# Performance work log

Measured on AMD Instinct MI355X. Metric: run time of the kernel, lower is better.

The kernel has to match this reference:

```python
import jax, jax.numpy as jnp
import numpy as np

N_NODES = 50000
EPS = 1e-12  # F.normalize eps


def _gcn_layer(x, W, b, src, dst):
    # GCNConv(normalize=False): h = x @ W, then sum-aggregate messages from
    # source nodes into target nodes along edge_index, then add bias.
    h = x @ W
    agg = jax.ops.segment_sum(h[src], dst, num_segments=N_NODES)
    out = agg + b
    # F.normalize(p=2, dim=-1) then ReLU
    norm = jnp.linalg.norm(out, axis=-1, keepdims=True)
    out = out / jnp.maximum(norm, EPS)
    return jax.nn.relu(out)


def setup_inputs() -> dict:
    key = jax.random.key(0)
    ks = jax.random.split(key, 8)
    nfeat, nhid, nclass, n_edges = 128, 128, 40, 640000
    x = jax.random.normal(ks[0], (N_NODES, nfeat), dtype=jnp.float32)
    edge_index = jax.random.randint(ks[1], (2, n_edges), 0, N_NODES, dtype=jnp.int64)
    s = 1.0 / np.sqrt(nhid)
    return {
        "x": x,
        "edge_index": edge_index,
        "W1": jax.random.normal(ks[2], (nfeat, nhid), jnp.float32) * s,
        "b1": jnp.zeros((nhid,), jnp.float32),
        "W2": jax.random.normal(ks[3], (nhid, nhid), jnp.float32) * s,
        "b2": jnp.zeros((nhid,), jnp.float32),
        "W3": jax.random.normal(ks[4], (nhid, nhid), jnp.float32) * s,
        "b3": jnp.zeros((nhid,), jnp.float32),
        "W4": jax.random.normal(ks[5], (nhid, nhid), jnp.float32) * s,
        "b4": jnp.zeros((nhid,), jnp.float32),
        "Wl": jax.random.normal(ks[6], (nhid, nclass), jnp.float32) * s,
        "bl": jnp.zeros((nclass,), jnp.float32),
    }


def reference(x, edge_index, W1, b1, W2, b2, W3, b3, W4, b4, Wl, bl):
    src, dst = edge_index[0], edge_index[1]
    x1 = _gcn_layer(x, W1, b1, src, dst)
    x2 = _gcn_layer(x1, W2, b2, src, dst)
    x3 = _gcn_layer(x2, W3, b3, src, dst)
    x4 = _gcn_layer(x3, W4, b4, src, dst)
    logits = x4 @ Wl + bl
    probs = jax.nn.softmax(logits, axis=-1)
    return (logits, probs, x4)
```

## Files before the change

### kernel.cpp

```cpp
#include <hip/hip_runtime.h>
#include <hip/hip_bf16.h>
#include <hip/hip_fp16.h>
#include <math.h>

#define NFEAT 128
#define NCLASS 40

typedef __attribute__((ext_vector_type(8))) short frag_ab;
typedef __attribute__((ext_vector_type(4))) float frag_cd;

static __device__ inline unsigned short f2bf_rne(float f) {
    union { float f; unsigned u; } v;
    v.f = f;
    unsigned r = v.u + 0x7FFFu + ((v.u >> 16) & 1u);
    return (unsigned short)(r >> 16);
}
static __device__ inline float bf2f(unsigned short h) {
    union { unsigned u; float f; } v;
    v.u = ((unsigned)h) << 16;
    return v.f;
}


__global__ __launch_bounds__(256) void prep_kernel(const float* __restrict__ x,
                                                   __half* __restrict__ xh, int xc4,
                                                   const float* __restrict__ W0,
                                                   const float* __restrict__ W1,
                                                   const float* __restrict__ W2,
                                                   const float* __restrict__ W3,
                                                   short* __restrict__ whi,
                                                   short* __restrict__ wlo,
                                                   const int* __restrict__ dst,
                                                   int* __restrict__ cnt, int n_edges,
                                                   int convB) {
    int b = blockIdx.x;
    if (b < convB) {
        int i = b * 256 + threadIdx.x;
        if (i < xc4) {
            float4 v = ((const float4*)x)[i];
            ((__half2*)xh)[i * 2 + 0] = __floats2half2_rn(v.x, v.y);
            ((__half2*)xh)[i * 2 + 1] = __floats2half2_rn(v.z, v.w);
        }
    } else if (b < convB + 32) {
        int wb = b - convB;
        int layer = wb >> 3;
        const float* W = layer == 0 ? W0 : layer == 1 ? W1 : layer == 2 ? W2 : W3;
        short* h = whi + (size_t)layer * 16384;
        short* l = wlo + (size_t)layer * 16384;
        int idx = (wb & 7) * 256 + threadIdx.x;
        int lane = idx & 63;
        int t = (idx >> 6) & 7;
        int s = idx >> 9;
        int quad = lane >> 4;
        int n = lane & 15;
        int kbase = s * 32 + quad * 8;
        int col = t * 16 + n;
#pragma unroll
        for (int j = 0; j < 8; ++j) {
            float f = W[(size_t)(kbase + j) * NFEAT + col];
            unsigned short hb = f2bf_rne(f);
            unsigned short lb = f2bf_rne(f - bf2f(hb));
            h[(size_t)idx * 8 + j] = (short)hb;
            l[(size_t)idx * 8 + j] = (short)lb;
        }
    } else {
        int hb = b - convB - 32;
        int i = hb * 256 + threadIdx.x;
        int n4 = n_edges >> 2;
        if (i < n4) {
            int4 d = ((const int4*)dst)[i];
            atomicAdd(&cnt[d.x], 1);
            atomicAdd(&cnt[d.y], 1);
            atomicAdd(&cnt[d.z], 1);
            atomicAdd(&cnt[d.w], 1);
        }
        if (hb == 0 && threadIdx.x == 0) {
            for (int e = n4 << 2; e < n_edges; ++e) atomicAdd(&cnt[dst[e]], 1);
        }
    }
}


__global__ __launch_bounds__(256) void scan1_kernel(const int* __restrict__ cnt,
                                                    int* __restrict__ excl,
                                                    int* __restrict__ bsums, int n) {
    __shared__ int sd[256];
    int t = threadIdx.x;
    int i = blockIdx.x * 256 + t;
    int v = (i < n) ? cnt[i] : 0;
    sd[t] = v;
    __syncthreads();
#pragma unroll
    for (int off = 1; off < 256; off <<= 1) {
        int tmp = (t >= off) ? sd[t - off] : 0;
        __syncthreads();
        sd[t] += tmp;
        __syncthreads();
    }
    if (i < n) excl[i] = sd[t] - v;
    if (t == 255) bsums[blockIdx.x] = sd[255];
}

__global__ __launch_bounds__(256) void scan3_kernel(const int* __restrict__ excl,
                                                    const int* __restrict__ bsums,
                                                    int* __restrict__ row_ptr,
                                                    int* __restrict__ woff, int n, int nb) {
    __shared__ int sd[256];
    __shared__ int off_s, tot_s;
    int t = threadIdx.x;
    int v = (t < nb) ? bsums[t] : 0;
    sd[t] = v;
    __syncthreads();
#pragma unroll
    for (int off = 1; off < 256; off <<= 1) {
        int tmp = (t >= off) ? sd[t - off] : 0;
        __syncthreads();
        sd[t] += tmp;
        __syncthreads();
    }
    if (t == 0) {
        off_s = (blockIdx.x > 0) ? sd[blockIdx.x - 1] : 0;
        tot_s = sd[255];
    }
    __syncthreads();
    int i = blockIdx.x * 256 + t;
    if (i < n) {
        int val = excl[i] + off_s;
        row_ptr[i] = val;
        woff[i] = val;
    }
    if (i == 0) row_ptr[n] = tot_s;
}

__global__ __launch_bounds__(256) void scatter_kernel(const int* __restrict__ src,
                                                      const int* __restrict__ dst,
                                                      int* __restrict__ woff,
                                                      int* __restrict__ src_sorted, int n_edges) {
    int i = blockIdx.x * 256 + threadIdx.x;
    int n4 = n_edges >> 2;
    if (i < n4) {
        int4 d = ((const int4*)dst)[i];
        int4 s = ((const int4*)src)[i];
        int p0 = atomicAdd(&woff[d.x], 1);
        int p1 = atomicAdd(&woff[d.y], 1);
        int p2 = atomicAdd(&woff[d.z], 1);
        int p3 = atomicAdd(&woff[d.w], 1);
        src_sorted[p0] = s.x;
        src_sorted[p1] = s.y;
        src_sorted[p2] = s.z;
        src_sorted[p3] = s.w;
    }
    if (i == 0) {
        for (int e = n4 << 2; e < n_edges; ++e) {
            int p = atomicAdd(&woff[dst[e]], 1);
            src_sorted[p] = src[e];
        }
    }
}


__global__ __launch_bounds__(256) void gcn_fused_kernel(const __half* __restrict__ xin,
                                                        const int* __restrict__ row_ptr,
                                                        const int* __restrict__ src_sorted,
                                                        const short* __restrict__ whi,
                                                        const short* __restrict__ wlo,
                                                        const float* __restrict__ bias,
                                                        float* __restrict__ outf,
                                                        __half* __restrict__ outh, int M) {
    __shared__ float smem[64][132];
    __shared__ int ctr;
    int tid = threadIdx.x;
    int base = blockIdx.x * 64;
    if (tid == 0) ctr = 0;
    __syncthreads();

    {
        int c = tid & 15;
        int lane = tid & 63;
        const uint4* xp = (const uint4*)xin;
        for (;;) {
            int nl = 0;
            if ((lane & 15) == 0) nl = atomicAdd(&ctr, 1);
            nl = __shfl(nl, lane & 48);
            if (nl >= 64) break;
            int node = base + nl;
            float a[8];
#pragma unroll
            for (int i = 0; i < 8; ++i) a[i] = 0.f;
            int jb = 0, je = 0;
            if (node < M) { jb = row_ptr[node]; je = row_ptr[node + 1]; }
            int j = jb;
            for (; j + 3 < je; j += 4) {
                int s0 = src_sorted[j];
                int s1 = src_sorted[j + 1];
                int s2 = src_sorted[j + 2];
                int s3 = src_sorted[j + 3];
                uint4 r0 = xp[s0 * 16 + c];
                uint4 r1 = xp[s1 * 16 + c];
                uint4 r2 = xp[s2 * 16 + c];
                uint4 r3 = xp[s3 * 16 + c];
#pragma unroll
                for (int q = 0; q < 4; ++q) {
                    unsigned u0 = (&r0.x)[q], u1 = (&r1.x)[q], u2 = (&r2.x)[q], u3 = (&r3.x)[q];
                    float2 f0 = __half22float2(*(__half2*)&u0);
                    float2 f1 = __half22float2(*(__half2*)&u1);
                    float2 f2 = __half22float2(*(__half2*)&u2);
                    float2 f3 = __half22float2(*(__half2*)&u3);
                    a[q * 2 + 0] += f0.x + f1.x + f2.x + f3.x;
                    a[q * 2 + 1] += f0.y + f1.y + f2.y + f3.y;
                }
            }
            for (; j < je; ++j) {
                int s0 = src_sorted[j];
                uint4 r0 = xp[s0 * 16 + c];
#pragma unroll
                for (int q = 0; q < 4; ++q) {
                    unsigned u0 = (&r0.x)[q];
                    float2 f0 = __half22float2(*(__half2*)&u0);
                    a[q * 2 + 0] += f0.x;
                    a[q * 2 + 1] += f0.y;
                }
            }
            float4* wp = (float4*)&smem[nl][c * 8];
            wp[0] = make_float4(a[0], a[1], a[2], a[3]);
            wp[1] = make_float4(a[4], a[5], a[6], a[7]);
        }
    }
    __syncthreads();

    int wave = tid >> 6;
    int lane = tid & 63;
    int quad = lane >> 4;
    int n16 = lane & 15;
    int lrow = wave * 16 + n16;

    const frag_ab* WH = (const frag_ab*)whi;
    const frag_ab* WL = (const frag_ab*)wlo;

    frag_cd acc[8];
#pragma unroll
    for (int t = 0; t < 8; ++t) acc[t] = (frag_cd){0.f, 0.f, 0.f, 0.f};

#pragma unroll
    for (int s = 0; s < 4; ++s) {
        const float* ap = &smem[lrow][s * 32 + quad * 8];
        float4 v0 = *(const float4*)(ap);
        float4 v1 = *(const float4*)(ap + 4);
        float fv[8] = {v0.x, v0.y, v0.z, v0.w, v1.x, v1.y, v1.z, v1.w};
        frag_ab ah, al;
#pragma unroll
        for (int jj = 0; jj < 8; ++jj) {
            unsigned short hb = f2bf_rne(fv[jj]);
            ah[jj] = (short)hb;
            al[jj] = (short)f2bf_rne(fv[jj] - bf2f(hb));
        }
#pragma unroll
        for (int t = 0; t < 8; ++t) {
            frag_ab bh = WH[(s * 8 + t) * 64 + lane];
            frag_ab bl = WL[(s * 8 + t) * 64 + lane];
            acc[t] = __builtin_amdgcn_mfma_f32_16x16x32_bf16(ah, bh, acc[t], 0, 0, 0);
            acc[t] = __builtin_amdgcn_mfma_f32_16x16x32_bf16(ah, bl, acc[t], 0, 0, 0);
            acc[t] = __builtin_amdgcn_mfma_f32_16x16x32_bf16(al, bh, acc[t], 0, 0, 0);
        }
    }

    float ssq[4] = {0.f, 0.f, 0.f, 0.f};
#pragma unroll
    for (int t = 0; t < 8; ++t) {
        float bv = bias[t * 16 + n16];
#pragma unroll
        for (int r = 0; r < 4; ++r) {
            acc[t][r] += bv;
            ssq[r] += acc[t][r] * acc[t][r];
        }
    }
#pragma unroll
    for (int mask = 1; mask <= 8; mask <<= 1) {
#pragma unroll
        for (int r = 0; r < 4; ++r) ssq[r] += __shfl_xor(ssq[r], mask);
    }
    float inv[4];
#pragma unroll
    for (int r = 0; r < 4; ++r) inv[r] = 1.0f / fmaxf(sqrtf(ssq[r]), 1e-12f);

    int orow0 = base + wave * 16 + quad * 4;
#pragma unroll
    for (int r = 0; r < 4; ++r) {
        int orow = orow0 + r;
        if (orow < M) {
            if (outh) {
                __half* op = outh + (size_t)orow * NFEAT + n16;
#pragma unroll
                for (int t = 0; t < 8; ++t)
                    op[t * 16] = __float2half(fmaxf(acc[t][r] * inv[r], 0.f));
            } else {
                float* op = outf + (size_t)orow * NFEAT + n16;
#pragma unroll
                for (int t = 0; t < 8; ++t)
                    op[t * 16] = fmaxf(acc[t][r] * inv[r], 0.f);
            }
        }
    }
}


__global__ __launch_bounds__(256) void classifier_kernel(const float* __restrict__ x4,
                                                         const float* __restrict__ Wl,
                                                         const float* __restrict__ bl,
                                                         float* __restrict__ logits,
                                                         float* __restrict__ probs, int n_nodes) {
    int node = blockIdx.x * 256 + threadIdx.x;
    int nc = node < n_nodes ? node : n_nodes - 1;
    const float* row = x4 + (size_t)nc * NFEAT;

    float acc[NCLASS];
#pragma unroll
    for (int c = 0; c < NCLASS; ++c) acc[c] = bl[c];

    for (int k = 0; k < NFEAT; k += 4) {
        float4 a = *(const float4*)(row + k);
#pragma unroll
        for (int kk = 0; kk < 4; ++kk) {
            float av = (&a.x)[kk];
            const float* Wr = Wl + (k + kk) * NCLASS;
#pragma unroll
            for (int c = 0; c < NCLASS; ++c) acc[c] += av * Wr[c];
        }
    }

    float m = acc[0];
#pragma unroll
    for (int c = 1; c < NCLASS; ++c) m = fmaxf(m, acc[c]);
    float ex[NCLASS];
    float sum = 0.f;
#pragma unroll
    for (int c = 0; c < NCLASS; ++c) {
        ex[c] = __expf(acc[c] - m);
        sum += ex[c];
    }
    float is = 1.0f / sum;

    if (node < n_nodes) {
        float4* lo = (float4*)(logits + (size_t)node * NCLASS);
        float4* po = (float4*)(probs + (size_t)node * NCLASS);
#pragma unroll
        for (int c = 0; c < NCLASS; c += 4) {
            float4 lv, pv;
            lv.x = acc[c + 0]; lv.y = acc[c + 1]; lv.z = acc[c + 2]; lv.w = acc[c + 3];
            pv.x = ex[c + 0] * is; pv.y = ex[c + 1] * is; pv.z = ex[c + 2] * is; pv.w = ex[c + 3] * is;
            lo[c >> 2] = lv;
            po[c >> 2] = pv;
        }
    }
}


extern "C" void kernel_launch(void* const* d_in, const int* in_sizes, int n_in,
                              void* d_out, int out_size, void* d_ws, size_t ws_size,
                              hipStream_t stream) {
    const float* x  = (const float*)d_in[0];
    const int*   ei = (const int*)d_in[1];
    const float* W1 = (const float*)d_in[2];
    const float* b1 = (const float*)d_in[3];
    const float* W2 = (const float*)d_in[4];
    const float* b2 = (const float*)d_in[5];
    const float* W3 = (const float*)d_in[6];
    const float* b3 = (const float*)d_in[7];
    const float* W4 = (const float*)d_in[8];
    const float* b4 = (const float*)d_in[9];
    const float* Wl = (const float*)d_in[10];
    const float* bl = (const float*)d_in[11];

    const int n_nodes = in_sizes[0] / NFEAT;
    const int n_edges = in_sizes[1] / 2;
    const int* src = ei;
    const int* dst = ei + n_edges;

    float* out    = (float*)d_out;
    float* logits = out;
    float* probs  = out + (size_t)n_nodes * NCLASS;
    float* x4     = out + 2 * (size_t)n_nodes * NCLASS;

    char* ws = (char*)d_ws;
    size_t off = 0;
    auto wsalloc = [&](size_t bytes) -> void* {
        void* p = ws + off;
        off += (bytes + 255) & ~(size_t)255;
        return p;
    };
    __half* xh         = (__half*)wsalloc((size_t)n_nodes * NFEAT * sizeof(__half));
    __half* xh2        = (__half*)wsalloc((size_t)n_nodes * NFEAT * sizeof(__half));
    int*    row_ptr    = (int*)wsalloc(((size_t)n_nodes + 1) * sizeof(int));
    int*    woff       = (int*)wsalloc((size_t)n_nodes * sizeof(int));
    int*    cnt        = (int*)wsalloc((size_t)n_nodes * sizeof(int));
    int*    src_sorted = (int*)wsalloc((size_t)n_edges * sizeof(int));
    int     nbt        = (n_nodes + 255) / 256;
    int*    bsums      = (int*)wsalloc(((size_t)nbt + 1) * sizeof(int));
    short*  whi        = (short*)wsalloc((size_t)4 * 16384 * sizeof(short));
    short*  wlo        = (short*)wsalloc((size_t)4 * 16384 * sizeof(short));

    hipMemsetAsync(cnt, 0, (size_t)n_nodes * sizeof(int), stream);

    int xc4   = (n_nodes * NFEAT) / 4;
    int convB = (xc4 + 255) / 256;
    int e4b   = ((n_edges >> 2) + 255) / 256;
    prep_kernel<<<convB + 32 + e4b, 256, 0, stream>>>(x, xh, xc4,
                                                      W1, W2, W3, W4, whi, wlo,
                                                      dst, cnt, n_edges, convB);

    scan1_kernel<<<nbt, 256, 0, stream>>>(cnt, row_ptr , bsums, n_nodes);
    scan3_kernel<<<nbt, 256, 0, stream>>>(row_ptr, bsums, row_ptr, woff, n_nodes, nbt);
    scatter_kernel<<<e4b, 256, 0, stream>>>(src, dst, woff, src_sorted, n_edges);

    int gb = (n_nodes + 63) / 64;
    int cb = (n_nodes + 255) / 256;

    gcn_fused_kernel<<<gb, 256, 0, stream>>>(xh,  row_ptr, src_sorted, whi + 0 * 16384, wlo + 0 * 16384, b1, nullptr, xh2, n_nodes);
    gcn_fused_kernel<<<gb, 256, 0, stream>>>(xh2, row_ptr, src_sorted, whi + 1 * 16384, wlo + 1 * 16384, b2, nullptr, xh,  n_nodes);
    gcn_fused_kernel<<<gb, 256, 0, stream>>>(xh,  row_ptr, src_sorted, whi + 2 * 16384, wlo + 2 * 16384, b3, nullptr, xh2, n_nodes);
    gcn_fused_kernel<<<gb, 256, 0, stream>>>(xh2, row_ptr, src_sorted, whi + 3 * 16384, wlo + 3 * 16384, b4, x4, nullptr, n_nodes);

    classifier_kernel<<<cb, 256, 0, stream>>>(x4, Wl, bl, logits, probs, n_nodes);
}
```

Baseline: 347.8 us.

## Split fused aggregate+GEMM into column-sliced aggregation and separate MFMA GEMM kernels

Unfuses each GCN layer into an aggregation kernel and a GEMM kernel. The aggregation kernel splits the feature columns into four slices across blocks and spreads the edges of each node over four lane groups, then reduces them with shuffles. It writes the aggregate to an fp16 buffer, which the GEMM reads back from global memory. The aim is more parallelism and cache-friendlier gathers, at the cost of an extra fp16 round trip through memory, an extra launch per layer, and rounding the aggregate to fp16 before the GEMM.

Measured after the change: 437.7 us. 1.26x slower.

```diff
diff --git a/kernel.cpp b/kernel.cpp
--- a/kernel.cpp
+++ b/kernel.cpp
@@ -159,80 +159,78 @@
 }
 
 
-__global__ __launch_bounds__(256) void gcn_fused_kernel(const __half* __restrict__ xin,
-                                                        const int* __restrict__ row_ptr,
-                                                        const int* __restrict__ src_sorted,
+__global__ __launch_bounds__(256) void agg_cs_kernel(const __half* __restrict__ xin,
+                                                     const int* __restrict__ row_ptr,
+                                                     const int* __restrict__ src_sorted,
+                                                     __half* __restrict__ aggh, int n_nodes) {
+    int slice = blockIdx.x & 3;
+    int tile  = blockIdx.x >> 2;
+    int tid = threadIdx.x;
+    int qw  = tid >> 4;
+    int l   = tid & 15;
+    int sg  = l >> 2;
+    int l4  = l & 3;
+
+    const uint4* xp = (const uint4*)xin;
+    int cofs = slice * 4 + l4;
+
+#pragma unroll 1
+    for (int p = 0; p < 4; ++p) {
+        int node = tile * 64 + qw * 4 + p;
+        if (node >= n_nodes) continue;
+        int jb = row_ptr[node], je = row_ptr[node + 1];
+        float a[8];
+#pragma unroll
+        for (int i = 0; i < 8; ++i) a[i] = 0.f;
+        for (int j = jb; j < je; j += 4) {
+            int jj = j + sg;
+            if (jj < je) {
+                int s0 = src_sorted[jj];
+                uint4 r = xp[(size_t)s0 * 16 + cofs];
+#pragma unroll
+                for (int q = 0; q < 4; ++q) {
+                    unsigned u = (&r.x)[q];
+                    float2 f = __half22float2(*(__half2*)&u);
+                    a[q * 2 + 0] += f.x;
+                    a[q * 2 + 1] += f.y;
+                }
+            }
+        }
+#pragma unroll
+        for (int i = 0; i < 8; ++i) {
+            a[i] += __shfl_xor(a[i], 4);
+            a[i] += __shfl_xor(a[i], 8);
+        }
+        if (sg == 0) {
+            __half2 h0 = __floats2half2_rn(a[0], a[1]);
+            __half2 h1 = __floats2half2_rn(a[2], a[3]);
+            __half2 h2 = __floats2half2_rn(a[4], a[5]);
+            __half2 h3 = __floats2half2_rn(a[6], a[7]);
+            uint4 o;
+            o.x = *(unsigned*)&h0; o.y = *(unsigned*)&h1;
+            o.z = *(unsigned*)&h2; o.w = *(unsigned*)&h3;
+            ((uint4*)aggh)[(size_t)node * 16 + cofs] = o;
+        }
+    }
+}
+
+
+__global__ __launch_bounds__(256) void gemm_mfma_kernel(const __half* __restrict__ A,
                                                         const short* __restrict__ whi,
                                                         const short* __restrict__ wlo,
                                                         const float* __restrict__ bias,
                                                         float* __restrict__ outf,
                                                         __half* __restrict__ outh, int M) {
-    __shared__ float smem[64][132];
-    __shared__ int ctr;
     int tid = threadIdx.x;
-    int base = blockIdx.x * 64;
-    if (tid == 0) ctr = 0;
-    __syncthreads();
-
-    {
-        int c = tid & 15;
-        int lane = tid & 63;
-        const uint4* xp = (const uint4*)xin;
-        for (;;) {
-            int nl = 0;
-            if ((lane & 15) == 0) nl = atomicAdd(&ctr, 1);
-            nl = __shfl(nl, lane & 48);
-            if (nl >= 64) break;
-            int node = base + nl;
-            float a[8];
-#pragma unroll
-            for (int i = 0; i < 8; ++i) a[i] = 0.f;
-            int jb = 0, je = 0;
-            if (node < M) { jb = row_ptr[node]; je = row_ptr[node + 1]; }
-            int j = jb;
-            for (; j + 3 < je; j += 4) {
-                int s0 = src_sorted[j];
-                int s1 = src_sorted[j + 1];
-                int s2 = src_sorted[j + 2];
-                int s3 = src_sorted[j + 3];
-                uint4 r0 = xp[s0 * 16 + c];
-                uint4 r1 = xp[s1 * 16 + c];
-                uint4 r2 = xp[s2 * 16 + c];
-                uint4 r3 = xp[s3 * 16 + c];
-#pragma unroll
-                for (int q = 0; q < 4; ++q) {
-                    unsigned u0 = (&r0.x)[q], u1 = (&r1.x)[q], u2 = (&r2.x)[q], u3 = (&r3.x)[q];
-                    float2 f0 = __half22float2(*(__half2*)&u0);
-                    float2 f1 = __half22float2(*(__half2*)&u1);
-                    float2 f2 = __half22float2(*(__half2*)&u2);
-                    float2 f3 = __half22float2(*(__half2*)&u3);
-                    a[q * 2 + 0] += f0.x + f1.x + f2.x + f3.x;
-                    a[q * 2 + 1] += f0.y + f1.y + f2.y + f3.y;
-                }
-            }
-            for (; j < je; ++j) {
-                int s0 = src_sorted[j];
-                uint4 r0 = xp[s0 * 16 + c];
-#pragma unroll
-                for (int q = 0; q < 4; ++q) {
-                    unsigned u0 = (&r0.x)[q];
-                    float2 f0 = __half22float2(*(__half2*)&u0);
-                    a[q * 2 + 0] += f0.x;
-                    a[q * 2 + 1] += f0.y;
-                }
-            }
-            float4* wp = (float4*)&smem[nl][c * 8];
-            wp[0] = make_float4(a[0], a[1], a[2], a[3]);
-            wp[1] = make_float4(a[4], a[5], a[6], a[7]);
-        }
-    }
-    __syncthreads();
-
     int wave = tid >> 6;
     int lane = tid & 63;
     int quad = lane >> 4;
     int n16 = lane & 15;
-    int lrow = wave * 16 + n16;
+    int base = blockIdx.x * 64;
+
+    int arow = base + wave * 16 + n16;
+    int arc = arow < M ? arow : M - 1;
+    const __half* Ar = A + (size_t)arc * NFEAT;
 
     const frag_ab* WH = (const frag_ab*)whi;
     const frag_ab* WL = (const frag_ab*)wlo;
@@ -243,16 +241,18 @@
 
 #pragma unroll
     for (int s = 0; s < 4; ++s) {
-        const float* ap = &smem[lrow][s * 32 + quad * 8];
-        float4 v0 = *(const float4*)(ap);
-        float4 v1 = *(const float4*)(ap + 4);
-        float fv[8] = {v0.x, v0.y, v0.z, v0.w, v1.x, v1.y, v1.z, v1.w};
+        uint4 av = *(const uint4*)(Ar + s * 32 + quad * 8);
         frag_ab ah, al;
 #pragma unroll
-        for (int jj = 0; jj < 8; ++jj) {
-            unsigned short hb = f2bf_rne(fv[jj]);
-            ah[jj] = (short)hb;
-            al[jj] = (short)f2bf_rne(fv[jj] - bf2f(hb));
+        for (int q = 0; q < 4; ++q) {
+            unsigned u = (&av.x)[q];
+            float2 f = __half22float2(*(__half2*)&u);
+            unsigned short hb0 = f2bf_rne(f.x);
+            unsigned short hb1 = f2bf_rne(f.y);
+            ah[q * 2 + 0] = (short)hb0;
+            ah[q * 2 + 1] = (short)hb1;
+            al[q * 2 + 0] = (short)f2bf_rne(f.x - bf2f(hb0));
+            al[q * 2 + 1] = (short)f2bf_rne(f.y - bf2f(hb1));
         }
 #pragma unroll
         for (int t = 0; t < 8; ++t) {
@@ -390,6 +390,7 @@
     };
     __half* xh         = (__half*)wsalloc((size_t)n_nodes * NFEAT * sizeof(__half));
     __half* xh2        = (__half*)wsalloc((size_t)n_nodes * NFEAT * sizeof(__half));
+    __half* aggh       = (__half*)wsalloc((size_t)n_nodes * NFEAT * sizeof(__half));
     int*    row_ptr    = (int*)wsalloc(((size_t)n_nodes + 1) * sizeof(int));
     int*    woff       = (int*)wsalloc((size_t)n_nodes * sizeof(int));
     int*    cnt        = (int*)wsalloc((size_t)n_nodes * sizeof(int));
@@ -412,13 +413,19 @@
     scan3_kernel<<<nbt, 256, 0, stream>>>(row_ptr, bsums, row_ptr, woff, n_nodes, nbt);
     scatter_kernel<<<e4b, 256, 0, stream>>>(src, dst, woff, src_sorted, n_edges);
 
-    int gb = (n_nodes + 63) / 64;
+    int tiles = (n_nodes + 63) / 64;
+    int ab = tiles * 4;
+    int gb = tiles;
     int cb = (n_nodes + 255) / 256;
 
-    gcn_fused_kernel<<<gb, 256, 0, stream>>>(xh,  row_ptr, src_sorted, whi + 0 * 16384, wlo + 0 * 16384, b1, nullptr, xh2, n_nodes);
-    gcn_fused_kernel<<<gb, 256, 0, stream>>>(xh2, row_ptr, src_sorted, whi + 1 * 16384, wlo + 1 * 16384, b2, nullptr, xh,  n_nodes);
-    gcn_fused_kernel<<<gb, 256, 0, stream>>>(xh,  row_ptr, src_sorted, whi + 2 * 16384, wlo + 2 * 16384, b3, nullptr, xh2, n_nodes);
-    gcn_fused_kernel<<<gb, 256, 0, stream>>>(xh2, row_ptr, src_sorted, whi + 3 * 16384, wlo + 3 * 16384, b4, x4, nullptr, n_nodes);
+    agg_cs_kernel<<<ab, 256, 0, stream>>>(xh, row_ptr, src_sorted, aggh, n_nodes);
+    gemm_mfma_kernel<<<gb, 256, 0, stream>>>(aggh, whi + 0 * 16384, wlo + 0 * 16384, b1, nullptr, xh2, n_nodes);
+    agg_cs_kernel<<<ab, 256, 0, stream>>>(xh2, row_ptr, src_sorted, aggh, n_nodes);
+    gemm_mfma_kernel<<<gb, 256, 0, stream>>>(aggh, whi + 1 * 16384, wlo + 1 * 16384, b2, nullptr, xh, n_nodes);
+    agg_cs_kernel<<<ab, 256, 0, stream>>>(xh, row_ptr, src_sorted, aggh, n_nodes);
+    gemm_mfma_kernel<<<gb, 256, 0, stream>>>(aggh, whi + 2 * 16384, wlo + 2 * 16384, b3, nullptr, xh2, n_nodes);
+    agg_cs_kernel<<<ab, 256, 0, stream>>>(xh2, row_ptr, src_sorted, aggh, n_nodes);
+    gemm_mfma_kernel<<<gb, 256, 0, stream>>>(aggh, whi + 3 * 16384, wlo + 3 * 16384, b4, x4, nullptr, n_nodes);
 
     classifier_kernel<<<cb, 256, 0, stream>>>(x4, Wl, bl, logits, probs, n_nodes);
 }
```
